# Performance work log

Measured on AMD Instinct MI355X. Metric: run time of the kernel, lower is better.

## Reference

```python
import jax, jax.numpy as jnp
import numpy as np

# Model hyperparams (must match init_kwargs)
N_CATEGORIES = 1000
EMBED_DIM = 128
N_DEMAND = 8
HIDDEN = 128
B, L, N_ITEMS = 16, 50, 8192


def setup_inputs() -> dict:
    key = jax.random.key(0)
    ks = jax.random.split(key, 12)
    inp = {}
    inp["input"] = jax.random.randint(ks[0], (B, L), 0, N_CATEGORIES)
    inp["candidate_pool_category"] = jax.random.randint(ks[1], (N_ITEMS,), 0, N_CATEGORIES)
    inp["session_last_catgy_index"] = jax.random.randint(ks[2], (B,), 0, L)
    inp["mask_catgy"] = jnp.ones((B, L), dtype=jnp.float32)
    # Learned parameters (torch Linear stored as (in, out) so y = x @ W + b)
    emb = 0.02 * jax.random.normal(ks[3], (N_CATEGORIES, EMBED_DIM), dtype=jnp.float32)
    inp["emb_table"] = emb.at[0].set(0.0)  # padding_idx=0
    sd = 1.0 / np.sqrt(EMBED_DIM)
    sh = 1.0 / np.sqrt(HIDDEN)
    inp["Wd"] = sd * jax.random.normal(ks[4], (EMBED_DIM, N_DEMAND * HIDDEN), dtype=jnp.float32)
    inp["Wk"] = sd * jax.random.normal(ks[5], (EMBED_DIM, HIDDEN), dtype=jnp.float32)
    inp["bk"] = sd * jax.random.normal(ks[6], (HIDDEN,), dtype=jnp.float32)
    inp["W1"] = (1.0 / np.sqrt(2 * HIDDEN)) * jax.random.normal(ks[7], (2 * HIDDEN, HIDDEN), dtype=jnp.float32)
    inp["b1"] = sh * jax.random.normal(ks[8], (HIDDEN,), dtype=jnp.float32)
    inp["w_score"] = sh * jax.random.normal(ks[9], (HIDDEN,), dtype=jnp.float32)
    inp["Wc"] = sh * jax.random.normal(ks[10], (HIDDEN, N_CATEGORIES), dtype=jnp.float32)
    inp["bc"] = sh * jax.random.normal(ks[11], (N_CATEGORIES,), dtype=jnp.float32)
    return inp


def reference(input, candidate_pool_category, session_last_catgy_index, mask_catgy,
              emb_table, Wd, Wk, bk, W1, b1, w_score, Wc, bc):
    B_, L_ = input.shape
    h = Wk.shape[1]
    D = Wd.shape[1] // h

    emb = emb_table[input]                      # (B, L, d)  (dropout = identity at eval)
    emb_cand = emb_table[candidate_pool_category]  # (N, d)

    hidden_key = emb @ Wk + bk                  # (B, L, h)
    hidden_demand = (emb @ Wd).reshape(B_, L_, D, h)
    # demand_agg == 'exp': log(sum(exp(.), axis=seq))
    agg = jax.nn.logsumexp(hidden_demand, axis=1)   # (B, D, h)

    # demand similarity loss: mean off-diagonal cosine similarity between demands
    hn = agg / (jnp.linalg.norm(agg, axis=-1, keepdims=True) + 1e-12)
    sim = jnp.einsum('bdh,beh->bde', hn, hn)
    off = sim * (1.0 - jnp.eye(D, dtype=sim.dtype))
    demand_sim_loss = jnp.sum(off) / (B_ * D * (D - 1))

    hidden_key_cand = emb_cand @ Wk + bk        # (N, h)

    # MLP score: cat([demand, key]) @ W1 == demand @ W1[:h] + key @ W1[h:]
    Wd1, Wk1 = W1[:h], W1[h:]
    pd = agg @ Wd1                              # (B, D, h)
    pk = hidden_key @ Wk1                       # (B, L, h)
    s = jax.nn.relu(pd[:, None, :, :] + pk[:, :, None, :] + b1)  # (B, L, D, h)
    # torch does .view(B, D, L) on a contiguous (B, L, D) tensor -> raw reshape (kept faithful)
    demand_score = (s @ w_score).reshape(B_, D, L_)              # (B, D, L)

    pkc = hidden_key_cand @ Wk1                 # (N, h)
    sc = jax.nn.relu(pd[:, :, None, :] + pkc[None, None, :, :] + b1)  # (B, D, N, h)
    demand_score_candidate = sc @ w_score       # (B, D, N)

    # predict_catgy ('mlp'): linear head over aggregated demand (reconstructed; body truncated in source)
    catgy_score = agg @ Wc + bc                 # (B, D, n_categories)

    return (catgy_score, demand_score, demand_score_candidate, emb, emb_cand, demand_sim_loss)
```

## Files before the change

### kernel.cpp

```cpp
#include <hip/hip_runtime.h>
#include <hip/hip_bf16.h>

#define NB 16
#define NL 50
#define ND 8
#define NH 128
#define NC 1000
#define NI 8192

#define OFF_CAT  0
#define OFF_DS   128000
#define OFF_DSC  134400
#define OFF_EMB  1182976
#define OFF_EMBC 1285376
#define OFF_LOSS 2333952

#define WS_AGG   0
#define WS_PD2   16384
#define WS_PK    32768
#define WS_SPART 135168
#define WS_PKCT  217088

__global__ __launch_bounds__(256) void k_embed(
    const int* __restrict__ inp, const int* __restrict__ cand,
    const float* __restrict__ emb_table, const float* __restrict__ Wk,
    const float* __restrict__ bk, const float* __restrict__ W1,
    float* __restrict__ out_emb, float* __restrict__ out_embc,
    float* __restrict__ ws_pk, float* __restrict__ ws_pkcT,
    float* __restrict__ out_loss)
{
    const int t = threadIdx.x;
    const int c = t & 127, g = t >> 7;
    __shared__ __align__(16) float smem[4096];
    float* s_e = smem;
    float* s_h = smem + 2048;
    const float* __restrict__ Wk1 = W1 + 128 * 128;
    const float bkv = bk[c];

    if (blockIdx.x < 100) {
        if (blockIdx.x == 0 && t == 0) out_loss[0] = 0.f;
        const int r0 = blockIdx.x * 8;
        #pragma unroll
        for (int r = 0; r < 4; ++r) {
            const int gr = g * 4 + r;
            const int cat = inp[r0 + gr];
            const float v = emb_table[cat * 128 + c];
            s_e[gr * 128 + c] = v;
            out_emb[(r0 + gr) * 128 + c] = v;
        }
        __syncthreads();
        float acc[4] = {bkv, bkv, bkv, bkv};
        for (int k = 0; k < 128; k += 4) {
            const float w0 = Wk[(k + 0) * 128 + c], w1 = Wk[(k + 1) * 128 + c];
            const float w2 = Wk[(k + 2) * 128 + c], w3 = Wk[(k + 3) * 128 + c];
            #pragma unroll
            for (int r = 0; r < 4; ++r) {
                const float4 e4 = *reinterpret_cast<const float4*>(&s_e[(g * 4 + r) * 128 + k]);
                acc[r] = fmaf(e4.w, w3, fmaf(e4.z, w2, fmaf(e4.y, w1, fmaf(e4.x, w0, acc[r]))));
            }
        }
        #pragma unroll
        for (int r = 0; r < 4; ++r) s_h[(g * 4 + r) * 128 + c] = acc[r];
        __syncthreads();
        float pk[4] = {0.f, 0.f, 0.f, 0.f};
        for (int k = 0; k < 128; k += 4) {
            const float w0 = Wk1[(k + 0) * 128 + c], w1 = Wk1[(k + 1) * 128 + c];
            const float w2 = Wk1[(k + 2) * 128 + c], w3 = Wk1[(k + 3) * 128 + c];
            #pragma unroll
            for (int r = 0; r < 4; ++r) {
                const float4 h4 = *reinterpret_cast<const float4*>(&s_h[(g * 4 + r) * 128 + k]);
                pk[r] = fmaf(h4.w, w3, fmaf(h4.z, w2, fmaf(h4.y, w1, fmaf(h4.x, w0, pk[r]))));
            }
        }
        #pragma unroll
        for (int r = 0; r < 4; ++r) ws_pk[(r0 + g * 4 + r) * 128 + c] = pk[r];
    } else {
        const int i0 = (blockIdx.x - 100) * 16;
        #pragma unroll
        for (int r = 0; r < 8; ++r) {
            const int gr = g * 8 + r;
            const int cat = cand[i0 + gr];
            const float v = emb_table[cat * 128 + c];
            s_e[gr * 128 + c] = v;
            out_embc[(i0 + gr) * 128 + c] = v;
        }
        __syncthreads();
        float acc[8];
        #pragma unroll
        for (int r = 0; r < 8; ++r) acc[r] = bkv;
        for (int k = 0; k < 128; k += 4) {
            const float w0 = Wk[(k + 0) * 128 + c], w1 = Wk[(k + 1) * 128 + c];
            const float w2 = Wk[(k + 2) * 128 + c], w3 = Wk[(k + 3) * 128 + c];
            #pragma unroll
            for (int r = 0; r < 8; ++r) {
                const float4 e4 = *reinterpret_cast<const float4*>(&s_e[(g * 8 + r) * 128 + k]);
                acc[r] = fmaf(e4.w, w3, fmaf(e4.z, w2, fmaf(e4.y, w1, fmaf(e4.x, w0, acc[r]))));
            }
        }
        #pragma unroll
        for (int r = 0; r < 8; ++r) s_h[(g * 8 + r) * 128 + c] = acc[r];
        __syncthreads();
        #pragma unroll
        for (int r = 0; r < 8; ++r) acc[r] = 0.f;
        for (int k = 0; k < 128; k += 4) {
            const float w0 = Wk1[(k + 0) * 128 + c], w1 = Wk1[(k + 1) * 128 + c];
            const float w2 = Wk1[(k + 2) * 128 + c], w3 = Wk1[(k + 3) * 128 + c];
            #pragma unroll
            for (int r = 0; r < 8; ++r) {
                const float4 h4 = *reinterpret_cast<const float4*>(&s_h[(g * 8 + r) * 128 + k]);
                acc[r] = fmaf(h4.w, w3, fmaf(h4.z, w2, fmaf(h4.y, w1, fmaf(h4.x, w0, acc[r]))));
            }
        }
        __syncthreads();
        float* tb = smem;
        #pragma unroll
        for (int r = 0; r < 8; ++r) tb[(g * 8 + r) * 132 + c] = acc[r];
        __syncthreads();
        #pragma unroll
        for (int p = 0; p < 2; ++p) {
            const int h = p * 64 + (t >> 2);
            const int ib = (t & 3) * 4;
            const float4 v = make_float4(tb[(ib + 0) * 132 + h], tb[(ib + 1) * 132 + h],
                                         tb[(ib + 2) * 132 + h], tb[(ib + 3) * 132 + h]);
            *reinterpret_cast<float4*>(&ws_pkcT[(size_t)h * NI + i0 + ib]) = v;
        }
    }
}

__global__ __launch_bounds__(256) void k_dsum(
    const float* __restrict__ out_emb, const float* __restrict__ Wd,
    float* __restrict__ ws_spart)
{
    const int bx = blockIdx.x;
    const int bd = bx / 5, chunk = bx % 5;
    const int b = bd >> 3, d = bd & 7;
    const int t = threadIdx.x;
    const int c = t & 127, half = t >> 7;
    __shared__ __align__(16) float se[1280];
    __shared__ float ss[2][128];
    const float* __restrict__ src = out_emb + (b * NL + chunk * 10) * 128;
    for (int i = t; i < 1280; i += 256) se[i] = src[i];
    __syncthreads();
    const float* __restrict__ wp = Wd + d * 128 + c;
    float acc[5] = {0.f, 0.f, 0.f, 0.f, 0.f};
    const int l0 = half * 5;
    for (int k = 0; k < 128; k += 4) {
        const float w0 = wp[(k + 0) * 1024], w1 = wp[(k + 1) * 1024];
        const float w2 = wp[(k + 2) * 1024], w3 = wp[(k + 3) * 1024];
        #pragma unroll
        for (int li = 0; li < 5; ++li) {
            const float4 e4 = *reinterpret_cast<const float4*>(&se[(l0 + li) * 128 + k]);
            acc[li] = fmaf(e4.w, w3, fmaf(e4.z, w2, fmaf(e4.y, w1, fmaf(e4.x, w0, acc[li]))));
        }
    }
    float s = 0.f;
    #pragma unroll
    for (int li = 0; li < 5; ++li) s += expf(acc[li]);
    ss[half][c] = s;
    __syncthreads();
    if (half == 0)
        ws_spart[(bd * 5 + chunk) * 128 + c] = ss[0][c] + ss[1][c];
}

__global__ __launch_bounds__(256) void k_agg2(
    const float* __restrict__ ws_spart, const float* __restrict__ W1,
    const float* __restrict__ b1, const float* __restrict__ Wc,
    const float* __restrict__ bc, float* __restrict__ ws_agg,
    float* __restrict__ ws_pd2, float* __restrict__ out_cat)
{
    const int bd = blockIdx.x;
    const int t = threadIdx.x;
    const int c = t & 127, half = t >> 7;
    __shared__ __align__(16) float a_s[128];
    if (half == 0) {
        float s = 0.f;
        #pragma unroll
        for (int ch = 0; ch < 5; ++ch) s += ws_spart[(bd * 5 + ch) * 128 + c];
        const float av = logf(s);
        a_s[c] = av;
        ws_agg[bd * 128 + c] = av;
    }
    __syncthreads();
    if (half == 0) {
        float acc = b1[c];
        for (int k = 0; k < 128; k += 4) {
            acc = fmaf(a_s[k + 0], W1[(k + 0) * 128 + c], acc);
            acc = fmaf(a_s[k + 1], W1[(k + 1) * 128 + c], acc);
            acc = fmaf(a_s[k + 2], W1[(k + 2) * 128 + c], acc);
            acc = fmaf(a_s[k + 3], W1[(k + 3) * 128 + c], acc);
        }
        ws_pd2[bd * 128 + c] = acc;
    }
    float acc4[4];
    int   col4[4];
    #pragma unroll
    for (int j = 0; j < 4; ++j) {
        const int col = t + j * 256;
        col4[j] = (col < NC) ? col : (NC - 1);
        acc4[j] = bc[col4[j]];
    }
    for (int k = 0; k < 128; ++k) {
        const float av = a_s[k];
        const float* wr = Wc + (size_t)k * NC;
        #pragma unroll
        for (int j = 0; j < 4; ++j) acc4[j] = fmaf(av, wr[col4[j]], acc4[j]);
    }
    #pragma unroll
    for (int j = 0; j < 4; ++j) {
        const int col = t + j * 256;
        if (col < NC) out_cat[bd * NC + col] = acc4[j];
    }
}

__global__ __launch_bounds__(256) void k_scores(
    const float* __restrict__ ws_pd2, const float* __restrict__ ws_pkcT,
    const float* __restrict__ ws_pk, const float* __restrict__ ws_agg,
    const float* __restrict__ w_score, float* __restrict__ out_dsc,
    float* __restrict__ out_ds, float* __restrict__ out_loss)
{
    const int bx = blockIdx.x;
    const int t = threadIdx.x;
    __shared__ __align__(16) float pd_s[1024];
    __shared__ __align__(16) float aux[276];

    if (bx < 512) {
        const int i = (bx & 31) * 256 + t;
        const int r0 = (bx >> 5) * 8;
        for (int j = t; j < 8 * 128; j += 256) pd_s[j] = ws_pd2[r0 * 128 + j];
        if (t < 128) aux[t] = w_score[t];
        __syncthreads();
        float acc[8];
        #pragma unroll
        for (int r = 0; r < 8; ++r) acc[r] = 0.f;
        for (int h = 0; h < 128; h += 4) {
            const float pv0 = ws_pkcT[(size_t)(h + 0) * NI + i];
            const float pv1 = ws_pkcT[(size_t)(h + 1) * NI + i];
            const float pv2 = ws_pkcT[(size_t)(h + 2) * NI + i];
            const float pv3 = ws_pkcT[(size_t)(h + 3) * NI + i];
            const float4 w4 = *reinterpret_cast<const float4*>(&aux[h]);
            #pragma unroll
            for (int r = 0; r < 8; ++r) {
                const float4 p4 = *reinterpret_cast<const float4*>(&pd_s[r * 128 + h]);
                acc[r] = fmaf(fmaxf(p4.x + pv0, 0.f), w4.x, acc[r]);
                acc[r] = fmaf(fmaxf(p4.y + pv1, 0.f), w4.y, acc[r]);
                acc[r] = fmaf(fmaxf(p4.z + pv2, 0.f), w4.z, acc[r]);
                acc[r] = fmaf(fmaxf(p4.w + pv3, 0.f), w4.w, acc[r]);
            }
        }
        #pragma unroll
        for (int r = 0; r < 8; ++r) out_dsc[(size_t)(r0 + r) * NI + i] = acc[r];
    } else if (bx < 1312) {
        const int bl = bx - 512;
        const int b = bl / 50, l = bl % 50;
        const int c = t & 127, g = t >> 7;
        const int w = t >> 6, lane = t & 63;
        float* red = aux;
        const float pkv = ws_pk[bl * 128 + c];
        const float wv = w_score[c];
        #pragma unroll
        for (int r = 0; r < 4; ++r) {
            const int d = g * 4 + r;
            float v = fmaxf(ws_pd2[(b * 8 + d) * 128 + c] + pkv, 0.f) * wv;
            v += __shfl_down(v, 32); v += __shfl_down(v, 16); v += __shfl_down(v, 8);
            v += __shfl_down(v, 4);  v += __shfl_down(v, 2);  v += __shfl_down(v, 1);
            if (lane == 0) red[w * 4 + r] = v;
        }
        __syncthreads();
        if (t < 8) {
            const int gg = t >> 2, rr = t & 3;
            out_ds[b * 400 + l * 8 + t] = red[(2 * gg) * 4 + rr] + red[(2 * gg + 1) * 4 + rr];
        }
    } else {
        const int b = bx - 1312;
        const int c = t & 127, g = t >> 7;
        const int w = t >> 6, lane = t & 63;
        float* normp = aux;
        float* sp    = aux + 16;
        float* wred  = aux + 272;
        float a[4];
        #pragma unroll
        for (int r = 0; r < 4; ++r) a[r] = ws_agg[(b * 8 + g * 4 + r) * 128 + c];
        #pragma unroll
        for (int r = 0; r < 4; ++r) {
            float s = a[r] * a[r];
            s += __shfl_down(s, 32); s += __shfl_down(s, 16); s += __shfl_down(s, 8);
            s += __shfl_down(s, 4);  s += __shfl_down(s, 2);  s += __shfl_down(s, 1);
            if (lane == 0) normp[w * 4 + r] = s;
        }
        __syncthreads();
        float Sp = 0.f;
        #pragma unroll
        for (int r = 0; r < 4; ++r) {
            const float nsq = normp[(2 * g) * 4 + r] + normp[(2 * g + 1) * 4 + r];
            const float iv = 1.f / (sqrtf(nsq) + 1e-12f);
            Sp = fmaf(a[r], iv, Sp);
        }
        sp[g * 128 + c] = Sp;
        __syncthreads();
        float p = 0.f;
        if (t < 128) {
            const float S = sp[c] + sp[128 + c];
            p = S * S;
        }
        p += __shfl_down(p, 32); p += __shfl_down(p, 16); p += __shfl_down(p, 8);
        p += __shfl_down(p, 4);  p += __shfl_down(p, 2);  p += __shfl_down(p, 1);
        if (lane == 0) wred[w] = p;
        __syncthreads();
        if (t == 0) {
            float corr = 0.f;
            #pragma unroll
            for (int d = 0; d < 8; ++d) {
                const float nsq = normp[(2 * (d >> 2)) * 4 + (d & 3)] +
                                  normp[(2 * (d >> 2) + 1) * 4 + (d & 3)];
                const float iv = 1.f / (sqrtf(nsq) + 1e-12f);
                corr = fmaf(nsq, iv * iv, corr);
            }
            atomicAdd(out_loss,
                      (wred[0] + wred[1] + wred[2] + wred[3] - corr) * (1.0f / 896.0f));
        }
    }
}

extern "C" void kernel_launch(void* const* d_in, const int* in_sizes, int n_in,
                              void* d_out, int out_size, void* d_ws, size_t ws_size,
                              hipStream_t stream)
{
    const int*   input     = (const int*)d_in[0];
    const int*   cand      = (const int*)d_in[1];
    const float* emb_table = (const float*)d_in[4];
    const float* Wd        = (const float*)d_in[5];
    const float* Wk        = (const float*)d_in[6];
    const float* bk        = (const float*)d_in[7];
    const float* W1        = (const float*)d_in[8];
    const float* b1        = (const float*)d_in[9];
    const float* w_score   = (const float*)d_in[10];
    const float* Wc        = (const float*)d_in[11];
    const float* bc        = (const float*)d_in[12];

    float* out = (float*)d_out;
    float* out_cat  = out + OFF_CAT;
    float* out_ds   = out + OFF_DS;
    float* out_dsc  = out + OFF_DSC;
    float* out_emb  = out + OFF_EMB;
    float* out_embc = out + OFF_EMBC;
    float* out_loss = out + OFF_LOSS;

    float* ws       = (float*)d_ws;
    float* ws_agg   = ws + WS_AGG;
    float* ws_pd2   = ws + WS_PD2;
    float* ws_pk    = ws + WS_PK;
    float* ws_spart = ws + WS_SPART;
    float* ws_pkcT  = ws + WS_PKCT;

    k_embed<<<612, 256, 0, stream>>>(input, cand, emb_table, Wk, bk, W1,
                                     out_emb, out_embc, ws_pk, ws_pkcT, out_loss);
    k_dsum<<<640, 256, 0, stream>>>(out_emb, Wd, ws_spart);
    k_agg2<<<128, 256, 0, stream>>>(ws_spart, W1, b1, Wc, bc, ws_agg, ws_pd2, out_cat);
    k_scores<<<1328, 256, 0, stream>>>(ws_pd2, ws_pkcT, ws_pk, ws_agg, w_score,
                                       out_dsc, out_ds, out_loss);
}
```

Baseline: 140.0 us.

## Fold Wk·Wk1 into one precomputed matrix and merge kernels into prep/main/tail

A small prep kernel multiplies Wk by the key half of W1 (and bk by it) so the key and candidate projections become a single 128x128 matmul instead of two. The logsumexp-partial kernel is merged into the main embedding kernel, gathering embeddings directly, and the aggregation, catgy head, pd computation and score kernels are merged into one tail kernel that recomputes agg and pd per block. This cuts launches and halves the projection FLOPs, at the cost of redundant pd recomputation in many tail blocks and slightly different floating-point rounding from reassociation.

Measured after the change: 151.8 us. +8.4%, slower.

```diff
diff --git a/kernel.cpp b/kernel.cpp
--- a/kernel.cpp
+++ b/kernel.cpp
@@ -15,100 +15,112 @@
 #define OFF_EMBC 1285376
 #define OFF_LOSS 2333952
 
-#define WS_AGG   0
-#define WS_PD2   16384
-#define WS_PK    32768
-#define WS_SPART 135168
-#define WS_PKCT  217088
-
-__global__ __launch_bounds__(256) void k_embed(
+#define WS_SPART 0
+#define WS_PK    81920
+#define WS_PKCT  184320
+#define WS_WP    1232896
+#define WS_BP    1249280
+
+__global__ __launch_bounds__(128) void k_prep(
+    const float* __restrict__ Wk, const float* __restrict__ bk,
+    const float* __restrict__ W1, float* __restrict__ ws_wp,
+    float* __restrict__ ws_bp, float* __restrict__ out_loss)
+{
+    const int t = threadIdx.x;
+    const int bxx = blockIdx.x;
+    __shared__ float wk_s[256];
+    const float* __restrict__ Wk1 = W1 + 128 * 128;
+    if (bxx < 64) {
+        const int r0 = bxx * 2;
+        wk_s[t]       = Wk[r0 * 128 + t];
+        wk_s[128 + t] = Wk[(r0 + 1) * 128 + t];
+        __syncthreads();
+        float a0 = 0.f, a1 = 0.f;
+        for (int k = 0; k < 128; k += 4) {
+            #pragma unroll
+            for (int j = 0; j < 4; ++j) {
+                const float w = Wk1[(k + j) * 128 + t];
+                a0 = fmaf(wk_s[k + j], w, a0);
+                a1 = fmaf(wk_s[128 + k + j], w, a1);
+            }
+        }
+        ws_wp[r0 * 128 + t]       = a0;
+        ws_wp[(r0 + 1) * 128 + t] = a1;
+    } else {
+        wk_s[t] = bk[t];
+        __syncthreads();
+        float a0 = 0.f;
+        for (int k = 0; k < 128; k += 4) {
+            #pragma unroll
+            for (int j = 0; j < 4; ++j)
+                a0 = fmaf(wk_s[k + j], Wk1[(k + j) * 128 + t], a0);
+        }
+        ws_bp[t] = a0;
+        if (t == 0) out_loss[0] = 0.f;
+    }
+}
+
+__global__ __launch_bounds__(256) void k_main(
     const int* __restrict__ inp, const int* __restrict__ cand,
-    const float* __restrict__ emb_table, const float* __restrict__ Wk,
-    const float* __restrict__ bk, const float* __restrict__ W1,
+    const float* __restrict__ emb_table, const float* __restrict__ Wd,
+    const float* __restrict__ ws_wp, const float* __restrict__ ws_bp,
     float* __restrict__ out_emb, float* __restrict__ out_embc,
     float* __restrict__ ws_pk, float* __restrict__ ws_pkcT,
-    float* __restrict__ out_loss)
+    float* __restrict__ ws_spart)
 {
+    const int bx = blockIdx.x;
     const int t = threadIdx.x;
     const int c = t & 127, g = t >> 7;
-    __shared__ __align__(16) float smem[4096];
-    float* s_e = smem;
-    float* s_h = smem + 2048;
-    const float* __restrict__ Wk1 = W1 + 128 * 128;
-    const float bkv = bk[c];
-
-    if (blockIdx.x < 100) {
-        if (blockIdx.x == 0 && t == 0) out_loss[0] = 0.f;
-        const int r0 = blockIdx.x * 8;
+    __shared__ __align__(16) float smem[2176];
+
+    if (bx < 100) {
+        const int r0 = bx * 8;
+        float* e_s = smem;
         #pragma unroll
         for (int r = 0; r < 4; ++r) {
             const int gr = g * 4 + r;
             const int cat = inp[r0 + gr];
             const float v = emb_table[cat * 128 + c];
-            s_e[gr * 128 + c] = v;
+            e_s[gr * 128 + c] = v;
             out_emb[(r0 + gr) * 128 + c] = v;
         }
         __syncthreads();
-        float acc[4] = {bkv, bkv, bkv, bkv};
-        for (int k = 0; k < 128; k += 4) {
-            const float w0 = Wk[(k + 0) * 128 + c], w1 = Wk[(k + 1) * 128 + c];
-            const float w2 = Wk[(k + 2) * 128 + c], w3 = Wk[(k + 3) * 128 + c];
+        const float bpv = ws_bp[c];
+        float acc[4] = {bpv, bpv, bpv, bpv};
+        for (int k = 0; k < 128; k += 4) {
+            const float w0 = ws_wp[(k + 0) * 128 + c], w1 = ws_wp[(k + 1) * 128 + c];
+            const float w2 = ws_wp[(k + 2) * 128 + c], w3 = ws_wp[(k + 3) * 128 + c];
             #pragma unroll
             for (int r = 0; r < 4; ++r) {
-                const float4 e4 = *reinterpret_cast<const float4*>(&s_e[(g * 4 + r) * 128 + k]);
+                const float4 e4 = *reinterpret_cast<const float4*>(&e_s[(g * 4 + r) * 128 + k]);
                 acc[r] = fmaf(e4.w, w3, fmaf(e4.z, w2, fmaf(e4.y, w1, fmaf(e4.x, w0, acc[r]))));
             }
         }
         #pragma unroll
-        for (int r = 0; r < 4; ++r) s_h[(g * 4 + r) * 128 + c] = acc[r];
-        __syncthreads();
-        float pk[4] = {0.f, 0.f, 0.f, 0.f};
-        for (int k = 0; k < 128; k += 4) {
-            const float w0 = Wk1[(k + 0) * 128 + c], w1 = Wk1[(k + 1) * 128 + c];
-            const float w2 = Wk1[(k + 2) * 128 + c], w3 = Wk1[(k + 3) * 128 + c];
-            #pragma unroll
-            for (int r = 0; r < 4; ++r) {
-                const float4 h4 = *reinterpret_cast<const float4*>(&s_h[(g * 4 + r) * 128 + k]);
-                pk[r] = fmaf(h4.w, w3, fmaf(h4.z, w2, fmaf(h4.y, w1, fmaf(h4.x, w0, pk[r]))));
-            }
-        }
-        #pragma unroll
-        for (int r = 0; r < 4; ++r) ws_pk[(r0 + g * 4 + r) * 128 + c] = pk[r];
-    } else {
-        const int i0 = (blockIdx.x - 100) * 16;
+        for (int r = 0; r < 4; ++r) ws_pk[(r0 + g * 4 + r) * 128 + c] = acc[r];
+    } else if (bx < 612) {
+        const int i0 = (bx - 100) * 16;
+        float* e_s = smem;
         #pragma unroll
         for (int r = 0; r < 8; ++r) {
             const int gr = g * 8 + r;
             const int cat = cand[i0 + gr];
             const float v = emb_table[cat * 128 + c];
-            s_e[gr * 128 + c] = v;
+            e_s[gr * 128 + c] = v;
             out_embc[(i0 + gr) * 128 + c] = v;
         }
         __syncthreads();
+        const float bpv = ws_bp[c];
         float acc[8];
         #pragma unroll
-        for (int r = 0; r < 8; ++r) acc[r] = bkv;
-        for (int k = 0; k < 128; k += 4) {
-            const float w0 = Wk[(k + 0) * 128 + c], w1 = Wk[(k + 1) * 128 + c];
-            const float w2 = Wk[(k + 2) * 128 + c], w3 = Wk[(k + 3) * 128 + c];
+        for (int r = 0; r < 8; ++r) acc[r] = bpv;
+        for (int k = 0; k < 128; k += 4) {
+            const float w0 = ws_wp[(k + 0) * 128 + c], w1 = ws_wp[(k + 1) * 128 + c];
+            const float w2 = ws_wp[(k + 2) * 128 + c], w3 = ws_wp[(k + 3) * 128 + c];
             #pragma unroll
             for (int r = 0; r < 8; ++r) {
-                const float4 e4 = *reinterpret_cast<const float4*>(&s_e[(g * 8 + r) * 128 + k]);
+                const float4 e4 = *reinterpret_cast<const float4*>(&e_s[(g * 8 + r) * 128 + k]);
                 acc[r] = fmaf(e4.w, w3, fmaf(e4.z, w2, fmaf(e4.y, w1, fmaf(e4.x, w0, acc[r]))));
-            }
-        }
-        #pragma unroll
-        for (int r = 0; r < 8; ++r) s_h[(g * 8 + r) * 128 + c] = acc[r];
-        __syncthreads();
-        #pragma unroll
-        for (int r = 0; r < 8; ++r) acc[r] = 0.f;
-        for (int k = 0; k < 128; k += 4) {
-            const float w0 = Wk1[(k + 0) * 128 + c], w1 = Wk1[(k + 1) * 128 + c];
-            const float w2 = Wk1[(k + 2) * 128 + c], w3 = Wk1[(k + 3) * 128 + c];
-            #pragma unroll
-            for (int r = 0; r < 8; ++r) {
-                const float4 h4 = *reinterpret_cast<const float4*>(&s_h[(g * 8 + r) * 128 + k]);
-                acc[r] = fmaf(h4.w, w3, fmaf(h4.z, w2, fmaf(h4.y, w1, fmaf(h4.x, w0, acc[r]))));
             }
         }
         __syncthreads();
@@ -124,110 +136,84 @@
                                          tb[(ib + 2) * 132 + h], tb[(ib + 3) * 132 + h]);
             *reinterpret_cast<float4*>(&ws_pkcT[(size_t)h * NI + i0 + ib]) = v;
         }
+    } else {
+        const int idx = bx - 612;
+        const int bd = idx / 5, chunk = idx % 5;
+        const int b = bd >> 3, d = bd & 7;
+        const int half = g;
+        float* se = smem;
+        float* ss = smem + 1280;
+        for (int ii = t; ii < 1280; ii += 256) {
+            const int row = ii >> 7, col = ii & 127;
+            const int cat = inp[b * NL + chunk * 10 + row];
+            se[ii] = emb_table[cat * 128 + col];
+        }
+        __syncthreads();
+        const float* __restrict__ wp = Wd + d * 128 + c;
+        float acc[5] = {0.f, 0.f, 0.f, 0.f, 0.f};
+        const int l0 = half * 5;
+        for (int k = 0; k < 128; k += 4) {
+            const float w0 = wp[(k + 0) * 1024], w1 = wp[(k + 1) * 1024];
+            const float w2 = wp[(k + 2) * 1024], w3 = wp[(k + 3) * 1024];
+            #pragma unroll
+            for (int li = 0; li < 5; ++li) {
+                const float4 e4 = *reinterpret_cast<const float4*>(&se[(l0 + li) * 128 + k]);
+                acc[li] = fmaf(e4.w, w3, fmaf(e4.z, w2, fmaf(e4.y, w1, fmaf(e4.x, w0, acc[li]))));
+            }
+        }
+        float s = 0.f;
+        #pragma unroll
+        for (int li = 0; li < 5; ++li) s += expf(acc[li]);
+        ss[half * 128 + c] = s;
+        __syncthreads();
+        if (half == 0)
+            ws_spart[(bd * 5 + chunk) * 128 + c] = ss[c] + ss[128 + c];
     }
 }
 
-__global__ __launch_bounds__(256) void k_dsum(
-    const float* __restrict__ out_emb, const float* __restrict__ Wd,
-    float* __restrict__ ws_spart)
-{
-    const int bx = blockIdx.x;
-    const int bd = bx / 5, chunk = bx % 5;
-    const int b = bd >> 3, d = bd & 7;
-    const int t = threadIdx.x;
-    const int c = t & 127, half = t >> 7;
-    __shared__ __align__(16) float se[1280];
-    __shared__ float ss[2][128];
-    const float* __restrict__ src = out_emb + (b * NL + chunk * 10) * 128;
-    for (int i = t; i < 1280; i += 256) se[i] = src[i];
-    __syncthreads();
-    const float* __restrict__ wp = Wd + d * 128 + c;
-    float acc[5] = {0.f, 0.f, 0.f, 0.f, 0.f};
-    const int l0 = half * 5;
-    for (int k = 0; k < 128; k += 4) {
-        const float w0 = wp[(k + 0) * 1024], w1 = wp[(k + 1) * 1024];
-        const float w2 = wp[(k + 2) * 1024], w3 = wp[(k + 3) * 1024];
-        #pragma unroll
-        for (int li = 0; li < 5; ++li) {
-            const float4 e4 = *reinterpret_cast<const float4*>(&se[(l0 + li) * 128 + k]);
-            acc[li] = fmaf(e4.w, w3, fmaf(e4.z, w2, fmaf(e4.y, w1, fmaf(e4.x, w0, acc[li]))));
-        }
-    }
-    float s = 0.f;
-    #pragma unroll
-    for (int li = 0; li < 5; ++li) s += expf(acc[li]);
-    ss[half][c] = s;
-    __syncthreads();
-    if (half == 0)
-        ws_spart[(bd * 5 + chunk) * 128 + c] = ss[0][c] + ss[1][c];
-}
-
-__global__ __launch_bounds__(256) void k_agg2(
-    const float* __restrict__ ws_spart, const float* __restrict__ W1,
-    const float* __restrict__ b1, const float* __restrict__ Wc,
-    const float* __restrict__ bc, float* __restrict__ ws_agg,
-    float* __restrict__ ws_pd2, float* __restrict__ out_cat)
-{
-    const int bd = blockIdx.x;
-    const int t = threadIdx.x;
-    const int c = t & 127, half = t >> 7;
-    __shared__ __align__(16) float a_s[128];
-    if (half == 0) {
-        float s = 0.f;
-        #pragma unroll
-        for (int ch = 0; ch < 5; ++ch) s += ws_spart[(bd * 5 + ch) * 128 + c];
-        const float av = logf(s);
-        a_s[c] = av;
-        ws_agg[bd * 128 + c] = av;
-    }
-    __syncthreads();
-    if (half == 0) {
-        float acc = b1[c];
-        for (int k = 0; k < 128; k += 4) {
-            acc = fmaf(a_s[k + 0], W1[(k + 0) * 128 + c], acc);
-            acc = fmaf(a_s[k + 1], W1[(k + 1) * 128 + c], acc);
-            acc = fmaf(a_s[k + 2], W1[(k + 2) * 128 + c], acc);
-            acc = fmaf(a_s[k + 3], W1[(k + 3) * 128 + c], acc);
-        }
-        ws_pd2[bd * 128 + c] = acc;
-    }
-    float acc4[4];
-    int   col4[4];
-    #pragma unroll
-    for (int j = 0; j < 4; ++j) {
-        const int col = t + j * 256;
-        col4[j] = (col < NC) ? col : (NC - 1);
-        acc4[j] = bc[col4[j]];
-    }
-    for (int k = 0; k < 128; ++k) {
-        const float av = a_s[k];
-        const float* wr = Wc + (size_t)k * NC;
-        #pragma unroll
-        for (int j = 0; j < 4; ++j) acc4[j] = fmaf(av, wr[col4[j]], acc4[j]);
-    }
-    #pragma unroll
-    for (int j = 0; j < 4; ++j) {
-        const int col = t + j * 256;
-        if (col < NC) out_cat[bd * NC + col] = acc4[j];
-    }
-}
-
-__global__ __launch_bounds__(256) void k_scores(
-    const float* __restrict__ ws_pd2, const float* __restrict__ ws_pkcT,
-    const float* __restrict__ ws_pk, const float* __restrict__ ws_agg,
-    const float* __restrict__ w_score, float* __restrict__ out_dsc,
-    float* __restrict__ out_ds, float* __restrict__ out_loss)
+__global__ __launch_bounds__(256) void k_tail(
+    const float* __restrict__ ws_spart, const float* __restrict__ ws_pk,
+    const float* __restrict__ ws_pkcT, const float* __restrict__ W1,
+    const float* __restrict__ b1, const float* __restrict__ w_score,
+    const float* __restrict__ Wc, const float* __restrict__ bc,
+    float* __restrict__ out_cat, float* __restrict__ out_ds,
+    float* __restrict__ out_dsc, float* __restrict__ out_loss)
 {
     const int bx = blockIdx.x;
     const int t = threadIdx.x;
-    __shared__ __align__(16) float pd_s[1024];
-    __shared__ __align__(16) float aux[276];
+    __shared__ __align__(16) float smem[5408];
+    float* a_s  = smem;
+    float* pd_s = smem + 1024;
+    float* ws_s = smem + 2048;
+    float* pk_s = smem + 2176;
+    float* aux  = smem + 5376;
 
     if (bx < 512) {
+        const int b = bx >> 5;
+        const int r0 = b * 8;
         const int i = (bx & 31) * 256 + t;
-        const int r0 = (bx >> 5) * 8;
-        for (int j = t; j < 8 * 128; j += 256) pd_s[j] = ws_pd2[r0 * 128 + j];
-        if (t < 128) aux[t] = w_score[t];
+        for (int j = t; j < 1024; j += 256) {
+            const int row = j >> 7, cc = j & 127;
+            float s = 0.f;
+            #pragma unroll
+            for (int ch = 0; ch < 5; ++ch) s += ws_spart[((r0 + row) * 5 + ch) * 128 + cc];
+            a_s[j] = logf(s);
+        }
+        if (t < 128) ws_s[t] = w_score[t];
+        __syncthreads();
+        {
+            const int c = t & 127, g = t >> 7;
+            const float b1v = b1[c];
+            float acc[4] = {b1v, b1v, b1v, b1v};
+            for (int k = 0; k < 128; ++k) {
+                const float w1v = W1[k * 128 + c];
+                #pragma unroll
+                for (int r = 0; r < 4; ++r)
+                    acc[r] = fmaf(a_s[(g * 4 + r) * 128 + k], w1v, acc[r]);
+            }
+            #pragma unroll
+            for (int r = 0; r < 4; ++r) pd_s[(g * 4 + r) * 128 + c] = acc[r];
+        }
         __syncthreads();
         float acc[8];
         #pragma unroll
@@ -237,7 +223,7 @@
             const float pv1 = ws_pkcT[(size_t)(h + 1) * NI + i];
             const float pv2 = ws_pkcT[(size_t)(h + 2) * NI + i];
             const float pv3 = ws_pkcT[(size_t)(h + 3) * NI + i];
-            const float4 w4 = *reinterpret_cast<const float4*>(&aux[h]);
+            const float4 w4 = *reinterpret_cast<const float4*>(&ws_s[h]);
             #pragma unroll
             for (int r = 0; r < 8; ++r) {
                 const float4 p4 = *reinterpret_cast<const float4*>(&pd_s[r * 128 + h]);
@@ -249,37 +235,54 @@
         }
         #pragma unroll
         for (int r = 0; r < 8; ++r) out_dsc[(size_t)(r0 + r) * NI + i] = acc[r];
-    } else if (bx < 1312) {
-        const int bl = bx - 512;
-        const int b = bl / 50, l = bl % 50;
-        const int c = t & 127, g = t >> 7;
-        const int w = t >> 6, lane = t & 63;
-        float* red = aux;
-        const float pkv = ws_pk[bl * 128 + c];
-        const float wv = w_score[c];
-        #pragma unroll
-        for (int r = 0; r < 4; ++r) {
-            const int d = g * 4 + r;
-            float v = fmaxf(ws_pd2[(b * 8 + d) * 128 + c] + pkv, 0.f) * wv;
-            v += __shfl_down(v, 32); v += __shfl_down(v, 16); v += __shfl_down(v, 8);
-            v += __shfl_down(v, 4);  v += __shfl_down(v, 2);  v += __shfl_down(v, 1);
-            if (lane == 0) red[w * 4 + r] = v;
-        }
-        __syncthreads();
-        if (t < 8) {
-            const int gg = t >> 2, rr = t & 3;
-            out_ds[b * 400 + l * 8 + t] = red[(2 * gg) * 4 + rr] + red[(2 * gg + 1) * 4 + rr];
+    } else if (bx < 640) {
+        const int bd = bx - 512;
+        const int c = t & 127, half = t >> 7;
+        if (half == 0) {
+            float s = 0.f;
+            #pragma unroll
+            for (int ch = 0; ch < 5; ++ch) s += ws_spart[(bd * 5 + ch) * 128 + c];
+            a_s[c] = logf(s);
+        }
+        __syncthreads();
+        float acc4[4];
+        int   col4[4];
+        #pragma unroll
+        for (int j = 0; j < 4; ++j) {
+            const int col = t + j * 256;
+            col4[j] = (col < NC) ? col : (NC - 1);
+            acc4[j] = bc[col4[j]];
+        }
+        for (int k = 0; k < 128; ++k) {
+            const float av = a_s[k];
+            const float* wr = Wc + (size_t)k * NC;
+            #pragma unroll
+            for (int j = 0; j < 4; ++j) acc4[j] = fmaf(av, wr[col4[j]], acc4[j]);
+        }
+        #pragma unroll
+        for (int j = 0; j < 4; ++j) {
+            const int col = t + j * 256;
+            if (col < NC) out_cat[bd * NC + col] = acc4[j];
         }
     } else {
-        const int b = bx - 1312;
+        const int b = bx - 640;
         const int c = t & 127, g = t >> 7;
         const int w = t >> 6, lane = t & 63;
         float* normp = aux;
-        float* sp    = aux + 16;
-        float* wred  = aux + 272;
+        float* wred  = aux + 16;
+        float* sp    = pk_s;
+        for (int j = t; j < 1024; j += 256) {
+            const int row = j >> 7, cc = j & 127;
+            float s = 0.f;
+            #pragma unroll
+            for (int ch = 0; ch < 5; ++ch) s += ws_spart[((b * 8 + row) * 5 + ch) * 128 + cc];
+            a_s[j] = logf(s);
+        }
+        if (t < 128) ws_s[t] = w_score[t];
+        __syncthreads();
         float a[4];
         #pragma unroll
-        for (int r = 0; r < 4; ++r) a[r] = ws_agg[(b * 8 + g * 4 + r) * 128 + c];
+        for (int r = 0; r < 4; ++r) a[r] = a_s[(g * 4 + r) * 128 + c];
         #pragma unroll
         for (int r = 0; r < 4; ++r) {
             float s = a[r] * a[r];
@@ -317,6 +320,35 @@
             }
             atomicAdd(out_loss,
                       (wred[0] + wred[1] + wred[2] + wred[3] - corr) * (1.0f / 896.0f));
+        }
+        {
+            const float b1v = b1[c];
+            float acc[4] = {b1v, b1v, b1v, b1v};
+            for (int k = 0; k < 128; ++k) {
+                const float w1v = W1[k * 128 + c];
+                #pragma unroll
+                for (int r = 0; r < 4; ++r)
+                    acc[r] = fmaf(a_s[(g * 4 + r) * 128 + k], w1v, acc[r]);
+            }
+            #pragma unroll
+            for (int r = 0; r < 4; ++r) pd_s[(g * 4 + r) * 128 + c] = acc[r];
+        }
+        __syncthreads();
+        #pragma unroll
+        for (int ch2 = 0; ch2 < 2; ++ch2) {
+            const int l0 = ch2 * 25;
+            __syncthreads();
+            for (int ii = t; ii < 3200; ii += 256)
+                pk_s[ii] = ws_pk[(size_t)(b * NL + l0) * 128 + ii];
+            __syncthreads();
+            for (int pp = w; pp < 200; pp += 4) {
+                const int l = pp >> 3, d = pp & 7;
+                float v = fmaxf(pd_s[d * 128 + lane] + pk_s[l * 128 + lane], 0.f) * ws_s[lane]
+                        + fmaxf(pd_s[d * 128 + 64 + lane] + pk_s[l * 128 + 64 + lane], 0.f) * ws_s[64 + lane];
+                v += __shfl_down(v, 32); v += __shfl_down(v, 16); v += __shfl_down(v, 8);
+                v += __shfl_down(v, 4);  v += __shfl_down(v, 2);  v += __shfl_down(v, 1);
+                if (lane == 0) out_ds[b * 400 + (l0 + l) * 8 + d] = v;
+            }
         }
     }
 }
@@ -346,16 +378,15 @@
     float* out_loss = out + OFF_LOSS;
 
     float* ws       = (float*)d_ws;
-    float* ws_agg   = ws + WS_AGG;
-    float* ws_pd2   = ws + WS_PD2;
+    float* ws_spart = ws + WS_SPART;
     float* ws_pk    = ws + WS_PK;
-    float* ws_spart = ws + WS_SPART;
     float* ws_pkcT  = ws + WS_PKCT;
-
-    k_embed<<<612, 256, 0, stream>>>(input, cand, emb_table, Wk, bk, W1,
-                                     out_emb, out_embc, ws_pk, ws_pkcT, out_loss);
-    k_dsum<<<640, 256, 0, stream>>>(out_emb, Wd, ws_spart);
-    k_agg2<<<128, 256, 0, stream>>>(ws_spart, W1, b1, Wc, bc, ws_agg, ws_pd2, out_cat);
-    k_scores<<<1328, 256, 0, stream>>>(ws_pd2, ws_pkcT, ws_pk, ws_agg, w_score,
-                                       out_dsc, out_ds, out_loss);
+    float* ws_wp    = ws + WS_WP;
+    float* ws_bp    = ws + WS_BP;
+
+    k_prep<<<65, 128, 0, stream>>>(Wk, bk, W1, ws_wp, ws_bp, out_loss);
+    k_main<<<1252, 256, 0, stream>>>(input, cand, emb_table, Wd, ws_wp, ws_bp,
+                                     out_emb, out_embc, ws_pk, ws_pkcT, ws_spart);
+    k_tail<<<656, 256, 0, stream>>>(ws_spart, ws_pk, ws_pkcT, W1, b1, w_score,
+                                    Wc, bc, out_cat, out_ds, out_dsc, out_loss);
 }
```
